# Optimization experiments

Measured on AMD Instinct MI355X. Metric: run time of the kernel, lower is better.

The kernel has to match this reference:

```python
import jax, jax.numpy as jnp
import numpy as np
from jax import lax

D_MODEL = 128

def _pad_same(x, kh, kw):
    ph, pw = kh - 1, kw - 1
    return jnp.pad(x, ((0, 0), (0, 0), (ph // 2, ph - ph // 2), (pw // 2, pw - pw // 2)))

def _conv(x, w, b):
    y = lax.conv_general_dilated(x, w, (1, 1), 'VALID', dimension_numbers=('NCHW', 'OIHW', 'NCHW'))
    return y + b[None, :, None, None]

def _group_norm(x, g, b, groups, eps=1e-5):
    N, C, H, W = x.shape
    xr = x.reshape(N, groups, -1)
    m = xr.mean(axis=2, keepdims=True)
    v = xr.var(axis=2, keepdims=True)
    xn = ((xr - m) / jnp.sqrt(v + eps)).reshape(N, C, H, W)
    return xn * g[None, :, None, None] + b[None, :, None, None]

def _maxpool(x, kh, kw):
    return lax.reduce_window(x, -jnp.inf, lax.max, (1, 1, kh, kw), (1, 1, kh, kw), 'VALID')

def _l2norm(x, axis):
    # torch F.normalize(p=2): x / max(||x||, eps)
    return x / jnp.maximum(jnp.linalg.norm(x, axis=axis, keepdims=True), 1e-12)

def _pos_encoding(S, d):
    pos = jnp.arange(S, dtype=jnp.float32)[:, None]
    div = jnp.exp(jnp.arange(0, d, 2, dtype=jnp.float32) * (-float(np.log(10000.0)) / d))
    pe = jnp.zeros((S, d), dtype=jnp.float32)
    pe = pe.at[:, 0::2].set(jnp.sin(pos * div)).at[:, 1::2].set(jnp.cos(pos * div))
    return pe

def setup_inputs() -> dict:
    key = jax.random.key(0)
    ks = jax.random.split(key, 16)
    def w(k, shape, fan_in):
        return jax.random.normal(k, shape, dtype=jnp.float32) * (1.0 / np.sqrt(fan_in))
    return {
        'x': jax.random.normal(ks[0], (1, 1024, 72, 64), dtype=jnp.float32),
        'conv1_w': w(ks[1], (32, 1, 6, 4), 1 * 6 * 4),
        'conv1_b': jnp.zeros((32,), jnp.float32),
        'gn1_g': jnp.ones((32,), jnp.float32), 'gn1_b': jnp.zeros((32,), jnp.float32),
        'conv2_w': w(ks[2], (64, 32, 6, 4), 32 * 6 * 4),
        'conv2_b': jnp.zeros((64,), jnp.float32),
        'gn2_g': jnp.ones((64,), jnp.float32), 'gn2_b': jnp.zeros((64,), jnp.float32),
        'conv3_w': w(ks[3], (128, 64, 6, 4), 64 * 6 * 4),
        'conv3_b': jnp.zeros((128,), jnp.float32),
        'gn3_g': jnp.ones((128,), jnp.float32), 'gn3_b': jnp.zeros((128,), jnp.float32),
        'fc1_w': w(ks[4], (128, 1024), 1024),
        'fc1_b': jnp.zeros((128,), jnp.float32),
        'wq': w(ks[5], (128, 128), 128), 'bq': jnp.zeros((128,), jnp.float32),
        'wk': w(ks[6], (128, 128), 128), 'bk': jnp.zeros((128,), jnp.float32),
        'wv': w(ks[7], (128, 128), 128), 'bv': jnp.zeros((128,), jnp.float32),
    }

def reference(x, conv1_w, conv1_b, gn1_g, gn1_b, conv2_w, conv2_b, gn2_g, gn2_b,
              conv3_w, conv3_b, gn3_g, gn3_b, fc1_w, fc1_b, wq, bq, wk, bk, wv, bv):
    selu = jax.nn.selu
    # x: [1, S, 72, 64] -> transpose(0,1): [S, 1, 72, 64] (S frames, 1 channel)
    h = jnp.transpose(x, (1, 0, 2, 3))
    h = _maxpool(_group_norm(selu(_conv(_pad_same(h, 6, 4), conv1_w, conv1_b)), gn1_g, gn1_b, 32), 2, 4)
    h = _maxpool(_group_norm(selu(_conv(_pad_same(h, 6, 4), conv2_w, conv2_b)), gn2_g, gn2_b, 32), 3, 4)
    h = _maxpool(_group_norm(selu(_conv(_pad_same(h, 6, 4), conv3_w, conv3_b)), gn3_g, gn3_b, 32), 3, 2)
    e = h.reshape(h.shape[0], -1)                       # [S, 1024]
    e = _l2norm(selu(e @ fc1_w.T + fc1_b), axis=1)      # [S, 128]
    S = e.shape[0]
    q = selu(e @ wq.T + bq)
    k = selu(e @ wk.T + bk)
    v = selu(e @ wv.T + bv)
    k_pos = k + _pos_encoding(S, D_MODEL)               # PE added to K only
    attn = jax.nn.softmax((q @ k_pos.T) / jnp.sqrt(jnp.float32(D_MODEL)), axis=-1)  # [S, S]
    # torch F.normalize default dim=1 on [1,S,D] -> normalize over the sequence axis
    out = _l2norm(attn @ v, axis=0) + e
    ea = _l2norm(out, axis=0)                           # [S, 128]
    # pairwise L2 distances (self-similarity matrix), then 1 - d/max(d)
    sq = jnp.sum(ea * ea, axis=1)
    d2 = jnp.maximum(sq[:, None] + sq[None, :] - 2.0 * (ea @ ea.T), 0.0)
    d = jnp.sqrt(d2 + 1e-12)
    return 1.0 - d / jnp.max(d)
```

## Files before the change

kernel.cpp:

```cpp
#include <hip/hip_runtime.h>
#include <hip/hip_bf16.h>
#include <math.h>

#define SELU_SCALE 1.0507009873554805f
#define SELU_SA    1.7580993408473766f

typedef __attribute__((ext_vector_type(8))) short short8;
typedef __attribute__((ext_vector_type(4))) short short4v;
typedef __attribute__((ext_vector_type(4))) float f32x4;

__device__ __forceinline__ float selu_f(float x){
    return x > 0.f ? SELU_SCALE * x : fmaf(SELU_SA, __expf(x), -SELU_SA);
}

__device__ __forceinline__ unsigned short bfc(float v){
    __hip_bfloat16 h = __float2bfloat16(v);
    return __builtin_bit_cast(unsigned short, h);
}
__device__ __forceinline__ float f_bf(unsigned short u){
    unsigned int x = ((unsigned int)u) << 16;
    return __builtin_bit_cast(float, x);
}

__device__ __forceinline__ float warp_max(float v){
    #pragma unroll
    for(int o=32;o>0;o>>=1) v = fmaxf(v,__shfl_down(v,o,64));
    return v;
}

__global__ void k_prep(const float* __restrict__ f1w, const float* __restrict__ wq,
                       const float* __restrict__ wk, const float* __restrict__ wv,
                       const float* __restrict__ w1, const float* __restrict__ w2,
                       const float* __restrict__ w3,
                       float* __restrict__ wt, float* __restrict__ wqt,
                       float* __restrict__ wkt, float* __restrict__ wvt,
                       short* __restrict__ w1bf, short* __restrict__ w2bf,
                       short* __restrict__ w3bf){
    int idx = blockIdx.x*256 + threadIdx.x;
    if(idx < 131072){ int r = idx >> 10, cc = idx & 1023; wt[cc*128 + r] = f1w[idx]; return; }
    idx -= 131072;
    if(idx < 16384){ int r = idx >> 7, cc = idx & 127; wqt[cc*128 + r] = wq[idx]; return; }
    idx -= 16384;
    if(idx < 16384){ int r = idx >> 7, cc = idx & 127; wkt[cc*128 + r] = wk[idx]; return; }
    idx -= 16384;
    if(idx < 16384){ int r = idx >> 7, cc = idx & 127; wvt[cc*128 + r] = wv[idx]; return; }
    idx -= 16384;
    if(idx < 49152){
        int t = idx >> 11, rem = idx & 2047;
        int oc = rem >> 5, ic = rem & 31;
        w2bf[idx] = (short)bfc(w2[oc*768 + ic*24 + t]);
        return;
    }
    idx -= 49152;
    if(idx < 196608){
        int t = idx >> 13, rem = idx & 8191;
        int oc = rem >> 6, ic = rem & 63;
        w3bf[idx] = (short)bfc(w3[oc*1536 + ic*24 + t]);
        return;
    }
    idx -= 196608;
    if(idx < 1024){
        int oc = idx >> 5, k = idx & 31;
        w1bf[idx] = (k < 24) ? (short)bfc(w1[oc*24 + k]) : (short)0;
    }
}

__global__ __launch_bounds__(1024,1) void k_conv1m(
    const float* __restrict__ x, const short* __restrict__ w1bf,
    const float* __restrict__ bias, const float* __restrict__ g,
    const float* __restrict__ be, unsigned short* __restrict__ out)
{
    int s = blockIdx.x, tid = threadIdx.x;
    int l = tid & 63, wv = tid >> 6;
    int c = l & 15, qr = l >> 4;
    __shared__ char smem[128752];
    short* sdup = (short*)smem;
    char* pmaxb = smem + 41712;
    char* pminb = smem + 83184;
    float* sredf = (float*)(smem + 124656);
    __shared__ float scsh[64];

    const float* xs = x + (size_t)s*4608;
    for(int i = tid; i < 5056; i += 1024){
        int yp = i >> 6, xx = i & 63;
        unsigned long long pk = 0ull;
        if(yp >= 2 && yp < 74){
            const float* row = xs + (yp-2)*64;
            #pragma unroll
            for(int t=0;t<4;t++){
                int cp = xx + t;
                float f = (cp>=1 && cp<65) ? row[cp-1] : 0.f;
                pk |= (unsigned long long)bfc(f) << (16*t);
            }
        }
        *(unsigned long long*)((char*)sdup + yp*528 + (xx&3)*128 + (xx>>2)*8) = pk;
    }
    short8 a0 = *(const short8*)(w1bf + c*32 + qr*8);
    short8 a1 = *(const short8*)(w1bf + (16+c)*32 + qr*8);
    float bias8[8];
    #pragma unroll
    for(int t=0;t<2;t++)
        #pragma unroll
        for(int r=0;r<4;r++) bias8[t*4+r] = bias[t*16 + qr*4 + r];
    float ssum8[8], ssq8[8];
    #pragma unroll
    for(int i=0;i<8;i++){ ssum8[i]=0.f; ssq8[i]=0.f; }
    __syncthreads();

    int nu, py0;
    if(wv < 4){ nu = 3; py0 = wv*3; } else { nu = 2; py0 = 12 + (wv-4)*2; }
    #pragma unroll 1
    for(int u=0; u<nu; u++){
        int py = py0 + u;
        float pmx[8], pmn[8];
        #pragma unroll
        for(int i=0;i<8;i++){ pmx[i]=-INFINITY; pmn[i]=INFINITY; }
        #pragma unroll
        for(int off=0; off<4; off++){
            const char* bb = (const char*)sdup + off*128 + c*8;
            #pragma unroll
            for(int rr=0; rr<2; rr++){
                int y = py*2 + rr;
                short4v lo = *(const short4v*)(bb + (y+2*qr)*528);
                short4v hi = *(const short4v*)(bb + (y+2*qr+1)*528);
                short8 bfrag = __builtin_shufflevector(lo, hi, 0,1,2,3,4,5,6,7);
                f32x4 d0 = __builtin_amdgcn_mfma_f32_16x16x32_bf16(a0, bfrag, (f32x4){0.f,0.f,0.f,0.f}, 0,0,0);
                f32x4 d1 = __builtin_amdgcn_mfma_f32_16x16x32_bf16(a1, bfrag, (f32x4){0.f,0.f,0.f,0.f}, 0,0,0);
                #pragma unroll
                for(int r=0;r<4;r++){
                    float v0 = selu_f(d0[r] + bias8[r]);
                    float v1 = selu_f(d1[r] + bias8[4+r]);
                    ssum8[r]   += v0; ssq8[r]   = fmaf(v0,v0,ssq8[r]);
                    ssum8[4+r] += v1; ssq8[4+r] = fmaf(v1,v1,ssq8[4+r]);
                    pmx[r]   = fmaxf(pmx[r],   v0); pmn[r]   = fminf(pmn[r],   v0);
                    pmx[4+r] = fmaxf(pmx[4+r], v1); pmn[4+r] = fminf(pmn[4+r], v1);
                }
            }
        }
        int base = (py*16 + c)*72;
        #pragma unroll
        for(int t=0;t<2;t++){
            unsigned long long mpk=0ull, npk=0ull;
            #pragma unroll
            for(int r=0;r<4;r++){
                mpk |= (unsigned long long)bfc(pmx[t*4+r]) << (16*r);
                npk |= (unsigned long long)bfc(pmn[t*4+r]) << (16*r);
            }
            *(unsigned long long*)(pmaxb + base + t*32 + qr*8) = mpk;
            *(unsigned long long*)(pminb + base + t*32 + qr*8) = npk;
        }
    }
    #pragma unroll
    for(int off=1; off<16; off<<=1){
        #pragma unroll
        for(int i=0;i<8;i++){
            ssum8[i] += __shfl_xor(ssum8[i], off);
            ssq8[i]  += __shfl_xor(ssq8[i],  off);
        }
    }
    if(c == 0){
        #pragma unroll
        for(int i=0;i<8;i++){
            sredf[((wv*4 + qr)*8 + i)*2]     = ssum8[i];
            sredf[((wv*4 + qr)*8 + i)*2 + 1] = ssq8[i];
        }
    }
    __syncthreads();
    if(tid < 32){
        int oc = tid;
        int t = oc >> 4, rem = oc & 15, q = rem >> 2, r = rem & 3;
        int i = t*4 + r;
        float sum=0.f, sq=0.f;
        for(int w=0; w<16; w++){
            sum += sredf[((w*4+q)*8+i)*2];
            sq  += sredf[((w*4+q)*8+i)*2+1];
        }
        float mean = sum*(1.f/4608.f);
        float var  = sq*(1.f/4608.f) - mean*mean;
        float inv  = rsqrtf(var + 1e-5f);
        float sc = g[oc]*inv;
        scsh[oc*2]   = sc;
        scsh[oc*2+1] = be[oc] - mean*sc;
    }
    __syncthreads();
    unsigned short* ob = out + (size_t)s*18432;
    for(int i = tid; i < 18432; i += 1024){
        int oc = i / 576, wpx = i - oc*576;
        float sc = scsh[oc*2], sh = scsh[oc*2+1];
        int boff = wpx*72 + oc*2;
        float vm = f_bf(*(unsigned short*)(pmaxb + boff));
        float vn = f_bf(*(unsigned short*)(pminb + boff));
        ob[i] = bfc(fmaf(sc, (sc >= 0.f) ? vm : vn, sh));
    }
}

__global__ __launch_bounds__(512,2) void k_conv23(
    const unsigned short* __restrict__ in, const short* __restrict__ w2bf,
    const float* __restrict__ b2, const float* __restrict__ g2,
    const float* __restrict__ e2,
    const short* __restrict__ w3bf,
    const float* __restrict__ b3, const float* __restrict__ g3,
    const float* __restrict__ e3, float* __restrict__ e0)
{
    int s = blockIdx.x, tid = threadIdx.x;
    int l = tid & 63, wv = tid >> 6;
    int ocp = wv >> 2, yq = wv & 3;
    int xc = l & 15, qr = l >> 4;
    __shared__ char cs[69888];
    short* sinb = (short*)cs;
    char*  s3in = cs + 52480;
    __shared__ float sredA[2][4][2][4][2][2];
    for(int i=tid;i<17472;i+=512) ((int*)cs)[i] = 0;
    __syncthreads();
    const unsigned short* ibase = in + (size_t)s*18432;
    #pragma unroll
    for(int h=0;h<2;h++){
        int ic = (wv*2+h)*2;
        #pragma unroll
        for(int k=0;k<9;k++){
            int px = l + 64*k;
            unsigned int v0 = ibase[ic*576 + px];
            unsigned int v1 = ibase[(ic+1)*576 + px];
            int R = (px>>4)+2, C = (px&15)+1;
            int key = (C>>1)&3;
            int q0 = ic>>3;
            int byteoff = (R*20+C)*64 + (((q0^key)&3)<<4) + (ic&7)*2;
            *(unsigned int*)((char*)sinb + byteoff) = v0 | (v1<<16);
        }
    }
    __syncthreads();
    f32x4 acc[2][9];
    #pragma unroll
    for(int o=0;o<2;o++)
        #pragma unroll
        for(int yt=0;yt<9;yt++) acc[o][yt] = (f32x4){0.f,0.f,0.f,0.f};
    const short8* wb = (const short8*)w2bf;
    int arow = ocp*32 + xc;
    short8 a0 = wb[arow*4 + qr];
    short8 a1 = wb[(arow+16)*4 + qr];
    char* sb = (char*)sinb;
    for(int tap=0; tap<24; tap++){
        short8 na0, na1;
        if(tap<23){
            na0 = wb[((tap+1)*64 + arow)*4 + qr];
            na1 = wb[((tap+1)*64 + arow + 16)*4 + qr];
        }
        int kh = tap>>2, kw = tap&3;
        int C = xc + kw;
        int cb = C*64 + (((qr ^ ((C>>1)&3))&3)<<4);
        int rb = (yq*9 + kh)*1280;
        #pragma unroll
        for(int yt=0;yt<9;yt++){
            short8 bf_ = *(const short8*)(sb + rb + yt*1280 + cb);
            acc[0][yt] = __builtin_amdgcn_mfma_f32_16x16x32_bf16(a0, bf_, acc[0][yt], 0,0,0);
            acc[1][yt] = __builtin_amdgcn_mfma_f32_16x16x32_bf16(a1, bf_, acc[1][yt], 0,0,0);
        }
        a0 = na0; a1 = na1;
    }
    #pragma unroll
    for(int o=0;o<2;o++){
        int ocb = (ocp*2+o)*16 + qr*4;
        float b0 = b2[ocb], b1 = b2[ocb+1], bb2 = b2[ocb+2], b3_ = b2[ocb+3];
        float s0=0,q0s=0,s1=0,q1=0;
        #pragma unroll
        for(int yt=0;yt<9;yt++){
            float v0=selu_f(acc[o][yt][0]+b0), v1=selu_f(acc[o][yt][1]+b1);
            float v2=selu_f(acc[o][yt][2]+bb2), v3=selu_f(acc[o][yt][3]+b3_);
            acc[o][yt][0]=v0; acc[o][yt][1]=v1; acc[o][yt][2]=v2; acc[o][yt][3]=v3;
            s0+=v0+v1; q0s+=v0*v0+v1*v1; s1+=v2+v3; q1+=v2*v2+v3*v3;
        }
        #pragma unroll
        for(int off=1;off<16;off<<=1){
            s0+=__shfl_xor(s0,off); q0s+=__shfl_xor(q0s,off);
            s1+=__shfl_xor(s1,off); q1+=__shfl_xor(q1,off);
        }
        if(xc==0){
            sredA[ocp][yq][o][qr][0][0]=s0; sredA[ocp][yq][o][qr][0][1]=q0s;
            sredA[ocp][yq][o][qr][1][0]=s1; sredA[ocp][yq][o][qr][1][1]=q1;
        }
    }
    __syncthreads();
    #pragma unroll
    for(int o=0;o<2;o++){
        #pragma unroll
        for(int grp=0;grp<2;grp++){
            float ts=0, tq=0;
            #pragma unroll
            for(int y2=0;y2<4;y2++){ ts += sredA[ocp][y2][o][qr][grp][0]; tq += sredA[ocp][y2][o][qr][grp][1]; }
            float mean = ts*(1.f/1152.f);
            float var  = tq*(1.f/1152.f) - mean*mean;
            float inv  = rsqrtf(var + 1e-5f);
            int oc0 = (ocp*2+o)*16 + qr*4 + grp*2;
            float sc0 = g2[oc0]*inv,   sh0 = e2[oc0]   - mean*sc0;
            float sc1 = g2[oc0+1]*inv, sh1 = e2[oc0+1] - mean*sc1;
            #pragma unroll
            for(int yt=0;yt<9;yt++){
                acc[o][yt][grp*2]   = acc[o][yt][grp*2]*sc0 + sh0;
                acc[o][yt][grp*2+1] = acc[o][yt][grp*2+1]*sc1 + sh1;
            }
        }
        #pragma unroll
        for(int r=0;r<4;r++){
            #pragma unroll
            for(int py=0;py<3;py++){
                float m = fmaxf(fmaxf(acc[o][3*py][r],acc[o][3*py+1][r]),acc[o][3*py+2][r]);
                m = fmaxf(m, __shfl_xor(m,1));
                m = fmaxf(m, __shfl_xor(m,2));
                if((xc&3)==0){
                    int oc = (ocp*2+o)*16 + qr*4 + r;
                    int R = yq*3 + py + 2;
                    int C = (xc>>2) + 1;
                    int key = ((R&1)<<2) | (C&3);
                    int q0 = oc>>3;
                    *(unsigned short*)(s3in + (R*8+C)*128 + (((q0^key)&7)<<4) + (oc&7)*2) = bfc(m);
                }
            }
        }
    }
    __syncthreads();
    int yl = xc >> 2, xl = xc & 3;
    f32x4 acc3[3];
    #pragma unroll
    for(int yt=0;yt<3;yt++) acc3[yt] = (f32x4){0.f,0.f,0.f,0.f};
    const short8* wb3 = (const short8*)w3bf;
    int arow3 = wv*16 + xc;
    short8 a3 = wb3[arow3*8 + qr];
    for(int t2=0; t2<48; t2++){
        short8 na3;
        if(t2<47){
            int nt = t2+1;
            na3 = wb3[((nt>>1)*128 + arow3)*8 + (nt&1)*4 + qr];
        }
        int tap = t2>>1, ks = t2&1;
        int kh = tap>>2, kw = tap&3;
        int C = xl + kw;
        int q0 = ks*4 + qr;
        #pragma unroll
        for(int yt=0;yt<3;yt++){
            int R = yt*4 + yl + kh;
            int key = ((R&1)<<2) | (C&3);
            short8 bf_ = *(const short8*)(s3in + (R*8+C)*128 + (((q0^key)&7)<<4));
            acc3[yt] = __builtin_amdgcn_mfma_f32_16x16x32_bf16(a3, bf_, acc3[yt], 0,0,0);
        }
        a3 = na3;
    }
    int ocb3 = wv*16 + qr*4;
    float c0 = b3[ocb3], c1 = b3[ocb3+1], c2 = b3[ocb3+2], c3 = b3[ocb3+3];
    float ssum=0.f, ssq=0.f;
    #pragma unroll
    for(int yt=0;yt<3;yt++){
        float v0=selu_f(acc3[yt][0]+c0), v1=selu_f(acc3[yt][1]+c1);
        float v2=selu_f(acc3[yt][2]+c2), v3=selu_f(acc3[yt][3]+c3);
        acc3[yt][0]=v0; acc3[yt][1]=v1; acc3[yt][2]=v2; acc3[yt][3]=v3;
        ssum += v0+v1+v2+v3; ssq += v0*v0+v1*v1+v2*v2+v3*v3;
    }
    #pragma unroll
    for(int off=1;off<16;off<<=1){ ssum+=__shfl_xor(ssum,off); ssq+=__shfl_xor(ssq,off); }
    float mean3 = ssum*(1.f/192.f);
    float var3  = ssq*(1.f/192.f) - mean3*mean3;
    float inv3  = rsqrtf(var3 + 1e-5f);
    float* scr = (float*)cs + wv*768;
    #pragma unroll
    for(int r=0;r<4;r++){
        int oc = ocb3 + r;
        float sc = g3[oc]*inv3, sh = e3[oc] - mean3*sc;
        #pragma unroll
        for(int yt=0;yt<3;yt++)
            scr[(qr*4+r)*48 + (yt*4+yl)*4 + xl] = acc3[yt][r]*sc + sh;
    }
    int oc_l = l>>2, pyw = l&3;
    const float* srd = (const float*)cs + wv*768 + oc_l*48;
    float* eo = e0 + (size_t)s*1024 + (wv*16 + oc_l)*8 + pyw*2;
    #pragma unroll
    for(int x2=0;x2<2;x2++){
        float m = srd[(pyw*3)*4 + x2*2];
        m = fmaxf(m, srd[(pyw*3)*4 + x2*2+1]);
        m = fmaxf(m, srd[(pyw*3+1)*4 + x2*2]);
        m = fmaxf(m, srd[(pyw*3+1)*4 + x2*2+1]);
        m = fmaxf(m, srd[(pyw*3+2)*4 + x2*2]);
        m = fmaxf(m, srd[(pyw*3+2)*4 + x2*2+1]);
        eo[x2] = m;
    }
}

__global__ __launch_bounds__(512) void k_fcqkv(
    const float* __restrict__ e0, const float* __restrict__ wt,
    const float* __restrict__ bias, float* __restrict__ et,
    const float* __restrict__ wqt, const float* __restrict__ bq,
    const float* __restrict__ wkt, const float* __restrict__ bk,
    const float* __restrict__ wvt, const float* __restrict__ bv,
    float* __restrict__ q, float* __restrict__ kp, float* __restrict__ v)
{
    int s0 = blockIdx.x*4, tid = threadIdx.x;
    int j = tid & 127, q4 = tid >> 7;
    __shared__ float se[4][1024];
    __shared__ float sp[4][4][128];
    __shared__ float sredn[4][2];
    __shared__ float se2[4][128];
    __shared__ float sp3[3][4][4][128];
    for(int i=tid;i<4096;i+=512){
        int sl = i >> 10, ii = i & 1023;
        se[sl][ii] = e0[(size_t)(s0+sl)*1024 + ii];
    }
    __syncthreads();
    float acc[4] = {0.f,0.f,0.f,0.f};
    const float* wp = wt + (size_t)q4*256*128 + j;
    const int ibase = q4*256;
    #pragma unroll 4
    for(int i=0;i<256;i++){
        float w = wp[(size_t)i*128];
        #pragma unroll
        for(int sl=0;sl<4;sl++) acc[sl] = fmaf(se[sl][ibase+i], w, acc[sl]);
    }
    #pragma unroll
    for(int sl=0;sl<4;sl++) sp[sl][q4][j] = acc[sl];
    __syncthreads();
    int sl2 = q4, lane = tid & 63, wv_ = tid >> 6;
    float vfc = selu_f(bias[j] + sp[sl2][0][j] + sp[sl2][1][j] + sp[sl2][2][j] + sp[sl2][3][j]);
    float a = vfc*vfc;
    #pragma unroll
    for(int o=1;o<64;o<<=1) a += __shfl_xor(a, o);
    if(lane==0) sredn[sl2][wv_&1] = a;
    __syncthreads();
    float den = fmaxf(sqrtf(sredn[sl2][0]+sredn[sl2][1]), 1e-12f);
    float ev = vfc/den;
    se2[sl2][j] = ev;
    et[(size_t)j*1024 + s0+sl2] = ev;
    __syncthreads();
    float aq[4]={0,0,0,0}, ak[4]={0,0,0,0}, av[4]={0,0,0,0};
    int i0b = q4*32;
    #pragma unroll 4
    for(int i=0;i<32;i++){
        float wqv = wqt[(i0b+i)*128 + j];
        float wkv = wkt[(i0b+i)*128 + j];
        float wvv = wvt[(i0b+i)*128 + j];
        #pragma unroll
        for(int sl=0;sl<4;sl++){
            float f = se2[sl][i0b+i];
            aq[sl] = fmaf(f, wqv, aq[sl]);
            ak[sl] = fmaf(f, wkv, ak[sl]);
            av[sl] = fmaf(f, wvv, av[sl]);
        }
    }
    #pragma unroll
    for(int sl=0;sl<4;sl++){
        sp3[0][sl][q4][j] = aq[sl];
        sp3[1][sl][q4][j] = ak[sl];
        sp3[2][sl][q4][j] = av[sl];
    }
    __syncthreads();
    float vq = selu_f(bq[j] + sp3[0][sl2][0][j]+sp3[0][sl2][1][j]+sp3[0][sl2][2][j]+sp3[0][sl2][3][j]);
    float vk = selu_f(bk[j] + sp3[1][sl2][0][j]+sp3[1][sl2][1][j]+sp3[1][sl2][2][j]+sp3[1][sl2][3][j]);
    float vv = selu_f(bv[j] + sp3[2][sl2][0][j]+sp3[2][sl2][1][j]+sp3[2][sl2][2][j]+sp3[2][sl2][3][j]);
    int i2 = j & ~1;
    float dv = __expf(-(float)i2 * 0.07195578412155481f);
    float ang = (float)(s0+sl2) * dv;
    float pe = (j & 1) ? cosf(ang) : sinf(ang);
    q[(size_t)(s0+sl2)*128+j]  = vq;
    kp[(size_t)(s0+sl2)*128+j] = vk + pe;
    v[(size_t)(s0+sl2)*128+j]  = vv;
}

__global__ __launch_bounds__(512) void k_attnav(
    const float* __restrict__ q, const float* __restrict__ kp,
    const float* __restrict__ v, float* __restrict__ avt)
{
    int s0 = blockIdx.x*4, tid = threadIdx.x;
    __shared__ float4 sq4[4][32];
    __shared__ float p[4][1024];
    __shared__ float spart[4][4][128];
    __shared__ float smx[4][2], ssm[4][2];
    ((float*)sq4)[tid] = q[(size_t)s0*128 + tid];
    __syncthreads();
    #pragma unroll
    for(int h=0;h<2;h++){
        int t = tid + h*512;
        const float4* kr = (const float4*)(kp + (size_t)t*128);
        float d[4] = {0.f,0.f,0.f,0.f};
        #pragma unroll 4
        for(int i=0;i<32;i++){
            float4 kv = kr[i];
            #pragma unroll
            for(int sl=0;sl<4;sl++){
                float4 qv = sq4[sl][i];
                d[sl] += kv.x*qv.x + kv.y*qv.y + kv.z*qv.z + kv.w*qv.w;
            }
        }
        #pragma unroll
        for(int sl=0;sl<4;sl++) p[sl][t] = d[sl]*0.08838834764831845f;
    }
    __syncthreads();
    int sl2 = tid>>7, t2 = tid&127, lane = tid&63, wv_ = tid>>6;
    float vals[8];
    float m = -INFINITY;
    #pragma unroll
    for(int k=0;k<8;k++){ vals[k] = p[sl2][t2 + k*128]; m = fmaxf(m, vals[k]); }
    #pragma unroll
    for(int o=1;o<64;o<<=1) m = fmaxf(m, __shfl_xor(m,o));
    if(lane==0) smx[sl2][wv_&1] = m;
    __syncthreads();
    m = fmaxf(smx[sl2][0], smx[sl2][1]);
    float lsum = 0.f;
    #pragma unroll
    for(int k=0;k<8;k++){ vals[k] = __expf(vals[k]-m); lsum += vals[k]; }
    #pragma unroll
    for(int o=1;o<64;o<<=1) lsum += __shfl_xor(lsum,o);
    if(lane==0) ssm[sl2][wv_&1] = lsum;
    __syncthreads();
    float invs = 1.f/(ssm[sl2][0]+ssm[sl2][1]);
    #pragma unroll
    for(int k=0;k<8;k++) p[sl2][t2+k*128] = vals[k]*invs;
    __syncthreads();
    int j = tid & 127, q4 = tid >> 7;
    float acc[4] = {0,0,0,0};
    int t0 = q4*256;
    #pragma unroll 2
    for(int t=t0;t<t0+256;t++){
        float vv = v[(size_t)t*128 + j];
        #pragma unroll
        for(int sl=0;sl<4;sl++) acc[sl] = fmaf(p[sl][t], vv, acc[sl]);
    }
    #pragma unroll
    for(int sl=0;sl<4;sl++) spart[sl][q4][j] = acc[sl];
    __syncthreads();
    avt[(size_t)j*1024 + s0+sl2] = spart[sl2][0][j]+spart[sl2][1][j]+spart[sl2][2][j]+spart[sl2][3][j];
}

__global__ __launch_bounds__(1024) void k_colpipe(
    const float* __restrict__ avt, const float* __restrict__ et, float* __restrict__ ea)
{
    int j = blockIdx.x, t = threadIdx.x;
    __shared__ float sred[16];
    int lane = t & 63, w = t >> 6;
    float vv = avt[(size_t)j*1024 + t];
    float ss = vv*vv;
    #pragma unroll
    for(int off=1;off<64;off<<=1) ss += __shfl_xor(ss,off);
    if(lane==0) sred[w]=ss;
    __syncthreads();
    float tot = 0.f;
    #pragma unroll
    for(int i=0;i<16;i++) tot += sred[i];
    float n1 = fmaxf(sqrtf(tot), 1e-12f);
    __syncthreads();
    float o = vv/n1 + et[(size_t)j*1024 + t];
    float ss2 = o*o;
    #pragma unroll
    for(int off=1;off<64;off<<=1) ss2 += __shfl_xor(ss2,off);
    if(lane==0) sred[w]=ss2;
    __syncthreads();
    float tot2 = 0.f;
    #pragma unroll
    for(int i=0;i<16;i++) tot2 += sred[i];
    float n2 = fmaxf(sqrtf(tot2), 1e-12f);
    ea[(size_t)t*128 + j] = o/n2;
}

__global__ __launch_bounds__(256) void k_gram(
    const float* __restrict__ ea,
    float* __restrict__ d2, unsigned int* __restrict__ maxbits)
{
    int j0 = blockIdx.x*32, i0 = blockIdx.y*32, tid = threadIdx.x;
    __shared__ float sa[32*128];
    __shared__ float sb[32*128];
    __shared__ float sredm[32];
    __shared__ float sqa[32], sqb[32];
    for(int idx=tid;idx<4096;idx+=256){
        sa[idx] = ea[(size_t)i0*128 + idx];
        sb[idx] = ea[(size_t)j0*128 + idx];
    }
    __syncthreads();
    {
        int r = tid>>3, seg = tid&7;
        const float* A = sa + r*128 + seg*16;
        const float* B = sb + r*128 + seg*16;
        float pa=0.f, pb=0.f;
        #pragma unroll
        for(int i=0;i<16;i++){ pa = fmaf(A[i],A[i],pa); pb = fmaf(B[i],B[i],pb); }
        #pragma unroll
        for(int o=1;o<8;o<<=1){ pa += __shfl_xor(pa,o); pb += __shfl_xor(pb,o); }
        if(seg==0){ sqa[r]=pa; sqb[r]=pb; }
    }
    __syncthreads();
    float lm = 0.f;
    #pragma unroll
    for(int k2=0;k2<4;k2++){
        int pp = tid + k2*256;
        int li = pp>>5, lj = pp&31;
        const float4* A = (const float4*)(sa + li*128);
        const float4* B = (const float4*)(sb + lj*128);
        float acc=0.f;
        #pragma unroll 8
        for(int i=0;i<32;i++){
            float4 a=A[i], b=B[i];
            acc += a.x*b.x + a.y*b.y + a.z*b.z + a.w*b.w;
        }
        float dd = fmaxf(sqa[li] + sqb[lj] - 2.f*acc, 0.f);
        d2[(size_t)(i0+li)*1024 + j0+lj] = dd;
        lm = fmaxf(lm, dd);
    }
    lm = warp_max(lm);
    __syncthreads();
    if((tid&63)==0) sredm[tid>>6]=lm;
    __syncthreads();
    if(tid==0){
        float mm = fmaxf(fmaxf(sredm[0],sredm[1]),fmaxf(sredm[2],sredm[3]));
        atomicMax(maxbits, __float_as_uint(mm));
    }
}

__global__ __launch_bounds__(256) void k_final(
    const float* __restrict__ d2, const unsigned int* __restrict__ maxbits, float* __restrict__ out)
{
    int idx = blockIdx.x*256 + threadIdx.x;
    float md = sqrtf(__uint_as_float(*maxbits) + 1e-12f);
    out[idx] = 1.f - sqrtf(d2[idx] + 1e-12f)/md;
}

extern "C" void kernel_launch(void* const* d_in, const int* in_sizes, int n_in,
                              void* d_out, int out_size, void* d_ws, size_t ws_size,
                              hipStream_t stream)
{
    const float* x   = (const float*)d_in[0];
    const float* c1w = (const float*)d_in[1];  const float* c1b = (const float*)d_in[2];
    const float* g1g = (const float*)d_in[3];  const float* g1b = (const float*)d_in[4];
    const float* c2w = (const float*)d_in[5];  const float* c2b = (const float*)d_in[6];
    const float* g2g = (const float*)d_in[7];  const float* g2b = (const float*)d_in[8];
    const float* c3w = (const float*)d_in[9];  const float* c3b = (const float*)d_in[10];
    const float* g3g = (const float*)d_in[11]; const float* g3b = (const float*)d_in[12];
    const float* f1w = (const float*)d_in[13]; const float* f1b = (const float*)d_in[14];
    const float* wq  = (const float*)d_in[15]; const float* bq  = (const float*)d_in[16];
    const float* wk  = (const float*)d_in[17]; const float* bk  = (const float*)d_in[18];
    const float* wv  = (const float*)d_in[19]; const float* bv  = (const float*)d_in[20];

    float* W = (float*)d_ws;
    float* e0   = W;
    float* eab  = W + 2228224;
    float* d2b  = W + 2359296;
    unsigned short* buf1 = (unsigned short*)(W + 4194304);
    float* wt   = W + 13631488;
    float* wqt  = W + 13762560;
    float* wkt  = W + 13778944;
    float* wvt  = W + 13795328;
    float* et   = W + 13811712;
    float* qb   = W + 13942784;
    float* kpb  = W + 14073856;
    float* vb   = W + 14204928;
    float* avt  = W + 14336000;
    unsigned int* maxb = (unsigned int*)(W + 14467072);
    short* w2bf = (short*)(W + 14467088);
    short* w3bf = (short*)(W + 14491664);
    short* w1bf = (short*)(W + 14589968);

    k_prep<<<1670,256,0,stream>>>(f1w, wq, wk, wv, c1w, c2w, c3w,
                                  wt, wqt, wkt, wvt, w1bf, w2bf, w3bf);

    k_conv1m<<<1024,1024,0,stream>>>(x, w1bf, c1b, g1g, g1b, buf1);
    k_conv23<<<1024,512,0,stream>>>(buf1, w2bf, c2b, g2g, g2b,
                                    w3bf, c3b, g3g, g3b, e0);

    k_fcqkv<<<256,512,0,stream>>>(e0, wt, f1b, et, wqt,bq, wkt,bk, wvt,bv, qb,kpb,vb);
    k_attnav<<<256,512,0,stream>>>(qb, kpb, vb, avt);

    hipMemsetAsync(maxb, 0, 4, stream);
    k_colpipe<<<128,1024,0,stream>>>(avt, et, eab);
    k_gram<<<dim3(32,32),256,0,stream>>>(eab, d2b, maxb);
    k_final<<<4096,256,0,stream>>>(d2b, maxb, (float*)d_out);
}
```

Before: 360.2 us.

## Restructure conv2/conv3 fused kernel to 12 waves with per-row output tiling

The fused conv2+conv3 kernel now launches 768 threads (12 waves) instead of 512. Each wave computes one pooled output row for all 64 conv2 channels, so the 3-row maxpool runs in registers, and the max/min trick folds the GroupNorm affine into the pool. Group statistics go through a shared reduction plus a per-group scale/shift table, and conv3 uses only 4 of the 12 waves with 32 channels each. This is meant to raise wave-level parallelism and cut per-wave accumulator registers, at the cost of more redundant B-fragment loads per wave, idle waves during conv3, and possibly lower occupancy with 768-thread blocks under the 2-block launch bound.

Measured after the change: 416.5 us. +15.6%, slower.

```diff
diff --git a/kernel.cpp b/kernel.cpp
--- a/kernel.cpp
+++ b/kernel.cpp
@@ -194,7 +194,7 @@
     }
 }
 
-__global__ __launch_bounds__(512,2) void k_conv23(
+__global__ __launch_bounds__(768,2) void k_conv23(
     const unsigned short* __restrict__ in, const short* __restrict__ w2bf,
     const float* __restrict__ b2, const float* __restrict__ g2,
     const float* __restrict__ e2,
@@ -204,182 +204,196 @@
 {
     int s = blockIdx.x, tid = threadIdx.x;
     int l = tid & 63, wv = tid >> 6;
-    int ocp = wv >> 2, yq = wv & 3;
     int xc = l & 15, qr = l >> 4;
     __shared__ char cs[69888];
     short* sinb = (short*)cs;
     char*  s3in = cs + 52480;
-    __shared__ float sredA[2][4][2][4][2][2];
-    for(int i=tid;i<17472;i+=512) ((int*)cs)[i] = 0;
+    __shared__ float sredB[12][64][2];
+    __shared__ float scsh2[128];
+    for(int i=tid;i<17472;i+=768) ((int*)cs)[i] = 0;
     __syncthreads();
     const unsigned short* ibase = in + (size_t)s*18432;
-    #pragma unroll
-    for(int h=0;h<2;h++){
-        int ic = (wv*2+h)*2;
-        #pragma unroll
-        for(int k=0;k<9;k++){
-            int px = l + 64*k;
-            unsigned int v0 = ibase[ic*576 + px];
-            unsigned int v1 = ibase[(ic+1)*576 + px];
-            int R = (px>>4)+2, C = (px&15)+1;
-            int key = (C>>1)&3;
-            int q0 = ic>>3;
-            int byteoff = (R*20+C)*64 + (((q0^key)&3)<<4) + (ic&7)*2;
-            *(unsigned int*)((char*)sinb + byteoff) = v0 | (v1<<16);
-        }
-    }
-    __syncthreads();
-    f32x4 acc[2][9];
-    #pragma unroll
-    for(int o=0;o<2;o++)
-        #pragma unroll
-        for(int yt=0;yt<9;yt++) acc[o][yt] = (f32x4){0.f,0.f,0.f,0.f};
+    for(int i=tid;i<9216;i+=768){
+        int icp = i/576, px = i - icp*576;
+        int ic = icp*2;
+        unsigned int v0 = ibase[ic*576 + px];
+        unsigned int v1 = ibase[(ic+1)*576 + px];
+        int R = (px>>4)+2, C = (px&15)+1;
+        int key = (C>>1)&3;
+        int q0 = ic>>3;
+        int byteoff = (R*20+C)*64 + (((q0^key)&3)<<4) + (ic&7)*2;
+        *(unsigned int*)((char*)sinb + byteoff) = v0 | (v1<<16);
+    }
+    __syncthreads();
+    f32x4 acc[4][3];
+    #pragma unroll
+    for(int t=0;t<4;t++)
+        #pragma unroll
+        for(int yt=0;yt<3;yt++) acc[t][yt] = (f32x4){0.f,0.f,0.f,0.f};
     const short8* wb = (const short8*)w2bf;
-    int arow = ocp*32 + xc;
-    short8 a0 = wb[arow*4 + qr];
-    short8 a1 = wb[(arow+16)*4 + qr];
+    short8 a[4], na[4];
+    #pragma unroll
+    for(int t=0;t<4;t++) a[t] = wb[(t*16 + xc)*4 + qr];
     char* sb = (char*)sinb;
+    int w3row = wv*3;
+    #pragma unroll 1
     for(int tap=0; tap<24; tap++){
-        short8 na0, na1;
         if(tap<23){
-            na0 = wb[((tap+1)*64 + arow)*4 + qr];
-            na1 = wb[((tap+1)*64 + arow + 16)*4 + qr];
+            #pragma unroll
+            for(int t=0;t<4;t++) na[t] = wb[((tap+1)*64 + t*16 + xc)*4 + qr];
         }
         int kh = tap>>2, kw = tap&3;
         int C = xc + kw;
         int cb = C*64 + (((qr ^ ((C>>1)&3))&3)<<4);
-        int rb = (yq*9 + kh)*1280;
-        #pragma unroll
-        for(int yt=0;yt<9;yt++){
-            short8 bf_ = *(const short8*)(sb + rb + yt*1280 + cb);
-            acc[0][yt] = __builtin_amdgcn_mfma_f32_16x16x32_bf16(a0, bf_, acc[0][yt], 0,0,0);
-            acc[1][yt] = __builtin_amdgcn_mfma_f32_16x16x32_bf16(a1, bf_, acc[1][yt], 0,0,0);
-        }
-        a0 = na0; a1 = na1;
-    }
-    #pragma unroll
-    for(int o=0;o<2;o++){
-        int ocb = (ocp*2+o)*16 + qr*4;
-        float b0 = b2[ocb], b1 = b2[ocb+1], bb2 = b2[ocb+2], b3_ = b2[ocb+3];
-        float s0=0,q0s=0,s1=0,q1=0;
-        #pragma unroll
-        for(int yt=0;yt<9;yt++){
-            float v0=selu_f(acc[o][yt][0]+b0), v1=selu_f(acc[o][yt][1]+b1);
-            float v2=selu_f(acc[o][yt][2]+bb2), v3=selu_f(acc[o][yt][3]+b3_);
-            acc[o][yt][0]=v0; acc[o][yt][1]=v1; acc[o][yt][2]=v2; acc[o][yt][3]=v3;
-            s0+=v0+v1; q0s+=v0*v0+v1*v1; s1+=v2+v3; q1+=v2*v2+v3*v3;
-        }
-        #pragma unroll
-        for(int off=1;off<16;off<<=1){
-            s0+=__shfl_xor(s0,off); q0s+=__shfl_xor(q0s,off);
-            s1+=__shfl_xor(s1,off); q1+=__shfl_xor(q1,off);
-        }
-        if(xc==0){
-            sredA[ocp][yq][o][qr][0][0]=s0; sredA[ocp][yq][o][qr][0][1]=q0s;
-            sredA[ocp][yq][o][qr][1][0]=s1; sredA[ocp][yq][o][qr][1][1]=q1;
-        }
-    }
-    __syncthreads();
-    #pragma unroll
-    for(int o=0;o<2;o++){
-        #pragma unroll
-        for(int grp=0;grp<2;grp++){
-            float ts=0, tq=0;
-            #pragma unroll
-            for(int y2=0;y2<4;y2++){ ts += sredA[ocp][y2][o][qr][grp][0]; tq += sredA[ocp][y2][o][qr][grp][1]; }
-            float mean = ts*(1.f/1152.f);
-            float var  = tq*(1.f/1152.f) - mean*mean;
-            float inv  = rsqrtf(var + 1e-5f);
-            int oc0 = (ocp*2+o)*16 + qr*4 + grp*2;
-            float sc0 = g2[oc0]*inv,   sh0 = e2[oc0]   - mean*sc0;
-            float sc1 = g2[oc0+1]*inv, sh1 = e2[oc0+1] - mean*sc1;
-            #pragma unroll
-            for(int yt=0;yt<9;yt++){
-                acc[o][yt][grp*2]   = acc[o][yt][grp*2]*sc0 + sh0;
-                acc[o][yt][grp*2+1] = acc[o][yt][grp*2+1]*sc1 + sh1;
-            }
-        }
+        #pragma unroll
+        for(int yt=0;yt<3;yt++){
+            short8 bf_ = *(const short8*)(sb + (w3row + yt + kh)*1280 + cb);
+            acc[0][yt] = __builtin_amdgcn_mfma_f32_16x16x32_bf16(a[0], bf_, acc[0][yt], 0,0,0);
+            acc[1][yt] = __builtin_amdgcn_mfma_f32_16x16x32_bf16(a[1], bf_, acc[1][yt], 0,0,0);
+            acc[2][yt] = __builtin_amdgcn_mfma_f32_16x16x32_bf16(a[2], bf_, acc[2][yt], 0,0,0);
+            acc[3][yt] = __builtin_amdgcn_mfma_f32_16x16x32_bf16(a[3], bf_, acc[3][yt], 0,0,0);
+        }
+        #pragma unroll
+        for(int t=0;t<4;t++) a[t] = na[t];
+    }
+    #pragma unroll
+    for(int t=0;t<4;t++){
         #pragma unroll
         for(int r=0;r<4;r++){
-            #pragma unroll
-            for(int py=0;py<3;py++){
-                float m = fmaxf(fmaxf(acc[o][3*py][r],acc[o][3*py+1][r]),acc[o][3*py+2][r]);
-                m = fmaxf(m, __shfl_xor(m,1));
-                m = fmaxf(m, __shfl_xor(m,2));
-                if((xc&3)==0){
-                    int oc = (ocp*2+o)*16 + qr*4 + r;
-                    int R = yq*3 + py + 2;
-                    int C = (xc>>2) + 1;
-                    int key = ((R&1)<<2) | (C&3);
-                    int q0 = oc>>3;
-                    *(unsigned short*)(s3in + (R*8+C)*128 + (((q0^key)&7)<<4) + (oc&7)*2) = bfc(m);
-                }
-            }
-        }
-    }
-    __syncthreads();
-    int yl = xc >> 2, xl = xc & 3;
-    f32x4 acc3[3];
-    #pragma unroll
-    for(int yt=0;yt<3;yt++) acc3[yt] = (f32x4){0.f,0.f,0.f,0.f};
-    const short8* wb3 = (const short8*)w3bf;
-    int arow3 = wv*16 + xc;
-    short8 a3 = wb3[arow3*8 + qr];
-    for(int t2=0; t2<48; t2++){
-        short8 na3;
-        if(t2<47){
-            int nt = t2+1;
-            na3 = wb3[((nt>>1)*128 + arow3)*8 + (nt&1)*4 + qr];
-        }
-        int tap = t2>>1, ks = t2&1;
-        int kh = tap>>2, kw = tap&3;
-        int C = xl + kw;
-        int q0 = ks*4 + qr;
-        #pragma unroll
-        for(int yt=0;yt<3;yt++){
-            int R = yt*4 + yl + kh;
-            int key = ((R&1)<<2) | (C&3);
-            short8 bf_ = *(const short8*)(s3in + (R*8+C)*128 + (((q0^key)&7)<<4));
-            acc3[yt] = __builtin_amdgcn_mfma_f32_16x16x32_bf16(a3, bf_, acc3[yt], 0,0,0);
-        }
-        a3 = na3;
-    }
-    int ocb3 = wv*16 + qr*4;
-    float c0 = b3[ocb3], c1 = b3[ocb3+1], c2 = b3[ocb3+2], c3 = b3[ocb3+3];
-    float ssum=0.f, ssq=0.f;
-    #pragma unroll
-    for(int yt=0;yt<3;yt++){
-        float v0=selu_f(acc3[yt][0]+c0), v1=selu_f(acc3[yt][1]+c1);
-        float v2=selu_f(acc3[yt][2]+c2), v3=selu_f(acc3[yt][3]+c3);
-        acc3[yt][0]=v0; acc3[yt][1]=v1; acc3[yt][2]=v2; acc3[yt][3]=v3;
-        ssum += v0+v1+v2+v3; ssq += v0*v0+v1*v1+v2*v2+v3*v3;
-    }
-    #pragma unroll
-    for(int off=1;off<16;off<<=1){ ssum+=__shfl_xor(ssum,off); ssq+=__shfl_xor(ssq,off); }
-    float mean3 = ssum*(1.f/192.f);
-    float var3  = ssq*(1.f/192.f) - mean3*mean3;
-    float inv3  = rsqrtf(var3 + 1e-5f);
-    float* scr = (float*)cs + wv*768;
-    #pragma unroll
-    for(int r=0;r<4;r++){
-        int oc = ocb3 + r;
-        float sc = g3[oc]*inv3, sh = e3[oc] - mean3*sc;
-        #pragma unroll
-        for(int yt=0;yt<3;yt++)
-            scr[(qr*4+r)*48 + (yt*4+yl)*4 + xl] = acc3[yt][r]*sc + sh;
-    }
-    int oc_l = l>>2, pyw = l&3;
-    const float* srd = (const float*)cs + wv*768 + oc_l*48;
-    float* eo = e0 + (size_t)s*1024 + (wv*16 + oc_l)*8 + pyw*2;
-    #pragma unroll
-    for(int x2=0;x2<2;x2++){
-        float m = srd[(pyw*3)*4 + x2*2];
-        m = fmaxf(m, srd[(pyw*3)*4 + x2*2+1]);
-        m = fmaxf(m, srd[(pyw*3+1)*4 + x2*2]);
-        m = fmaxf(m, srd[(pyw*3+1)*4 + x2*2+1]);
-        m = fmaxf(m, srd[(pyw*3+2)*4 + x2*2]);
-        m = fmaxf(m, srd[(pyw*3+2)*4 + x2*2+1]);
-        eo[x2] = m;
+            int oc = t*16 + qr*4 + r;
+            float bb = b2[oc];
+            float sv=0.f, qv=0.f;
+            #pragma unroll
+            for(int yt=0;yt<3;yt++){
+                float v = selu_f(acc[t][yt][r] + bb);
+                acc[t][yt][r] = v;
+                sv += v; qv = fmaf(v,v,qv);
+            }
+            #pragma unroll
+            for(int off=1;off<16;off<<=1){ sv += __shfl_xor(sv,off); qv += __shfl_xor(qv,off); }
+            if(xc==0){ sredB[wv][oc][0]=sv; sredB[wv][oc][1]=qv; }
+        }
+    }
+    __syncthreads();
+    if(tid < 32){
+        int gidx = tid;
+        int oc0 = gidx*2;
+        float sum=0.f, sq=0.f;
+        for(int w=0;w<12;w++){
+            sum += sredB[w][oc0][0] + sredB[w][oc0+1][0];
+            sq  += sredB[w][oc0][1] + sredB[w][oc0+1][1];
+        }
+        float mean = sum*(1.f/1152.f);
+        float var  = sq*(1.f/1152.f) - mean*mean;
+        float inv  = rsqrtf(var + 1e-5f);
+        #pragma unroll
+        for(int o2=0;o2<2;o2++){
+            int oc = oc0+o2;
+            float sc = g2[oc]*inv;
+            scsh2[oc*2]   = sc;
+            scsh2[oc*2+1] = e2[oc] - mean*sc;
+        }
+    }
+    __syncthreads();
+    #pragma unroll
+    for(int t=0;t<4;t++){
+        #pragma unroll
+        for(int r=0;r<4;r++){
+            int oc = t*16 + qr*4 + r;
+            float sc = scsh2[oc*2], sh = scsh2[oc*2+1];
+            float m = fmaxf(fmaxf(acc[t][0][r], acc[t][1][r]), acc[t][2][r]);
+            m = m*sc;
+            float mn = fminf(fminf(acc[t][0][r], acc[t][1][r]), acc[t][2][r]);
+            float vsel = (sc >= 0.f) ? m : mn*sc;
+            float pv = vsel + sh;
+            pv = fmaxf(pv, __shfl_xor(pv,1));
+            pv = fmaxf(pv, __shfl_xor(pv,2));
+            if((xc&3)==0){
+                int R = wv + 2;
+                int C = (xc>>2) + 1;
+                int key = ((R&1)<<2) | (C&3);
+                int q0 = oc>>3;
+                *(unsigned short*)(s3in + (R*8+C)*128 + (((q0^key)&7)<<4) + (oc&7)*2) = bfc(pv);
+            }
+        }
+    }
+    __syncthreads();
+    if(wv < 4){
+        int yl = xc >> 2, xl = xc & 3;
+        f32x4 acc3[2][3];
+        #pragma unroll
+        for(int o=0;o<2;o++)
+            #pragma unroll
+            for(int yt=0;yt<3;yt++) acc3[o][yt] = (f32x4){0.f,0.f,0.f,0.f};
+        const short8* wb3 = (const short8*)w3bf;
+        int ar0 = wv*32 + xc, ar1 = wv*32 + 16 + xc;
+        short8 a30 = wb3[ar0*8 + qr];
+        short8 a31 = wb3[ar1*8 + qr];
+        #pragma unroll 1
+        for(int t2=0; t2<48; t2++){
+            short8 n30, n31;
+            if(t2<47){
+                int nt = t2+1;
+                n30 = wb3[((nt>>1)*128 + ar0)*8 + (nt&1)*4 + qr];
+                n31 = wb3[((nt>>1)*128 + ar1)*8 + (nt&1)*4 + qr];
+            }
+            int tap = t2>>1, ks = t2&1;
+            int kh = tap>>2, kw = tap&3;
+            int C = xl + kw;
+            int q0 = ks*4 + qr;
+            #pragma unroll
+            for(int yt=0;yt<3;yt++){
+                int R = yt*4 + yl + kh;
+                int key = ((R&1)<<2) | (C&3);
+                short8 bf_ = *(const short8*)(s3in + (R*8+C)*128 + (((q0^key)&7)<<4));
+                acc3[0][yt] = __builtin_amdgcn_mfma_f32_16x16x32_bf16(a30, bf_, acc3[0][yt], 0,0,0);
+                acc3[1][yt] = __builtin_amdgcn_mfma_f32_16x16x32_bf16(a31, bf_, acc3[1][yt], 0,0,0);
+            }
+            a30 = n30; a31 = n31;
+        }
+        float* scr = (float*)cs + wv*1536;
+        #pragma unroll
+        for(int o=0;o<2;o++){
+            int ocb3 = wv*32 + o*16 + qr*4;
+            float c0 = b3[ocb3], c1 = b3[ocb3+1], c2 = b3[ocb3+2], c3 = b3[ocb3+3];
+            float ssum=0.f, ssq=0.f;
+            #pragma unroll
+            for(int yt=0;yt<3;yt++){
+                float v0=selu_f(acc3[o][yt][0]+c0), v1=selu_f(acc3[o][yt][1]+c1);
+                float v2=selu_f(acc3[o][yt][2]+c2), v3=selu_f(acc3[o][yt][3]+c3);
+                acc3[o][yt][0]=v0; acc3[o][yt][1]=v1; acc3[o][yt][2]=v2; acc3[o][yt][3]=v3;
+                ssum += v0+v1+v2+v3; ssq += v0*v0+v1*v1+v2*v2+v3*v3;
+            }
+            #pragma unroll
+            for(int off=1;off<16;off<<=1){ ssum+=__shfl_xor(ssum,off); ssq+=__shfl_xor(ssq,off); }
+            float mean3 = ssum*(1.f/192.f);
+            float var3  = ssq*(1.f/192.f) - mean3*mean3;
+            float inv3  = rsqrtf(var3 + 1e-5f);
+            #pragma unroll
+            for(int r=0;r<4;r++){
+                int oc = ocb3 + r;
+                float sc = g3[oc]*inv3, sh = e3[oc] - mean3*sc;
+                #pragma unroll
+                for(int yt=0;yt<3;yt++)
+                    scr[(o*16 + qr*4 + r)*48 + (yt*4+yl)*4 + xl] = acc3[o][yt][r]*sc + sh;
+            }
+        }
+    }
+    __syncthreads();
+    if(wv < 4){
+        int oc_l = l >> 1, x2 = l & 1;
+        const float* srd = (const float*)cs + wv*1536 + oc_l*48;
+        float* eo = e0 + (size_t)s*1024 + (wv*32 + oc_l)*8;
+        #pragma unroll
+        for(int py=0;py<4;py++){
+            float m = srd[(py*3)*4 + x2*2];
+            m = fmaxf(m, srd[(py*3)*4 + x2*2+1]);
+            m = fmaxf(m, srd[(py*3+1)*4 + x2*2]);
+            m = fmaxf(m, srd[(py*3+1)*4 + x2*2+1]);
+            m = fmaxf(m, srd[(py*3+2)*4 + x2*2]);
+            m = fmaxf(m, srd[(py*3+2)*4 + x2*2+1]);
+            eo[py*2 + x2] = m;
+        }
     }
 }
 
@@ -656,7 +670,7 @@
                                   wt, wqt, wkt, wvt, w1bf, w2bf, w3bf);
 
     k_conv1m<<<1024,1024,0,stream>>>(x, w1bf, c1b, g1g, g1b, buf1);
-    k_conv23<<<1024,512,0,stream>>>(buf1, w2bf, c2b, g2g, g2b,
+    k_conv23<<<1024,768,0,stream>>>(buf1, w2bf, c2b, g2g, g2b,
                                     w3bf, c3b, g3g, g3b, e0);
 
     k_fcqkv<<<256,512,0,stream>>>(e0, wt, f1b, et, wqt,bq, wkt,bk, wvt,bv, qb,kpb,vb);
```
